# Kernel tuning notes

Measured on AMD Instinct MI355X. Metric: run time of the kernel, lower is better.

Reference implementation:

```python
import jax, jax.numpy as jnp
import numpy as np

BS, D = 8192, 128
SIGMA = 16.0

def setup_inputs() -> dict:
    key = jax.random.key(0)
    x = jax.random.normal(key, (BS, D), dtype=jnp.float32)
    return {"x": x}

def reference(x) -> jnp.ndarray:
    # kernel[j, i] = exp(-||x_i - x_j||^2 / (2 sigma^2))  (symmetric RBF Gram matrix)
    # Computed via the ||a-b||^2 = |a|^2 + |b|^2 - 2 a.b GEMM trick instead of the
    # original O(bs) loop of slice/sub/sum ops (same math, fused form).
    sq = jnp.sum(x * x, axis=1)                      # [bs]
    d2 = sq[:, None] + sq[None, :] - 2.0 * (x @ x.T)  # [bs, bs]
    d2 = jnp.maximum(d2, 0.0)                         # clamp tiny negative fp error
    kernel = jnp.exp(-d2 / (2.0 * SIGMA * SIGMA))
    # symmetric degree normalization: D^{-1/2} K D^{-1/2}
    ds = 1.0 / jnp.sqrt(jnp.sum(kernel, axis=0))      # [bs]
    return kernel * (ds[:, None] * ds[None, :])
```

## Files before the change

### kernel.cpp

```cpp
#include <hip/hip_runtime.h>
#include <hip/hip_bf16.h>

#define BSZ 8192
#define DIM 128

typedef __attribute__((ext_vector_type(8))) short bf16x8;
typedef __attribute__((ext_vector_type(4))) float f32x4;

__device__ __forceinline__ ushort f32_to_bf16(float f) {
    unsigned u = __float_as_uint(f);
    u += 0x7FFF + ((u >> 16) & 1);
    return (ushort)(u >> 16);
}

__global__ __launch_bounds__(256) void prep_kernel(const float* __restrict__ x,
                                                   ushort* __restrict__ xb,
                                                   float* __restrict__ sq) {
    const int wid  = threadIdx.x >> 6;
    const int lane = threadIdx.x & 63;
    const int g    = blockIdx.x * 4 + wid;
    const int fr   = lane & 15;
    const int kg   = lane >> 4;
    const int row  = g * 16 + fr;

    float s = 0.f;
    #pragma unroll
    for (int kk = 0; kk < 4; ++kk) {
        const float* p = x + (size_t)row * DIM + kk * 32 + kg * 8;
        const float4 v0 = *reinterpret_cast<const float4*>(p);
        const float4 v1 = *reinterpret_cast<const float4*>(p + 4);
        s += v0.x * v0.x + v0.y * v0.y + v0.z * v0.z + v0.w * v0.w;
        s += v1.x * v1.x + v1.y * v1.y + v1.z * v1.z + v1.w * v1.w;
        bf16x8 b;
        b[0] = (short)f32_to_bf16(v0.x); b[1] = (short)f32_to_bf16(v0.y);
        b[2] = (short)f32_to_bf16(v0.z); b[3] = (short)f32_to_bf16(v0.w);
        b[4] = (short)f32_to_bf16(v1.x); b[5] = (short)f32_to_bf16(v1.y);
        b[6] = (short)f32_to_bf16(v1.z); b[7] = (short)f32_to_bf16(v1.w);
        *reinterpret_cast<bf16x8*>(xb + ((size_t)(g * 4 + kk) * 64 + lane) * 8) = b;
    }
    s += __shfl_xor(s, 16);
    s += __shfl_xor(s, 32);
    if (lane < 16) sq[row] = s;
}

template <int PHASE>
__global__ __launch_bounds__(256) void rbf_kernel(const ushort* __restrict__ xb,
                                                  const float* __restrict__ sq,
                                                  float* __restrict__ colsum,
                                                  float* __restrict__ out) {
    const int lane = threadIdx.x & 63;
    const int wid  = threadIdx.x >> 6;
    const int fr   = lane & 15;
    const int kg   = lane >> 4;

    const int bx = blockIdx.x & 63;
    const int by = blockIdx.x >> 6;
    const int row0 = by * 128 + (wid >> 1) * 64;
    const int col0 = bx * 128 + (wid & 1) * 64;
    const int ga = row0 >> 4;
    const int gb = col0 >> 4;

    f32x4 acc[4][4];
    #pragma unroll
    for (int mi = 0; mi < 4; ++mi)
        #pragma unroll
        for (int ni = 0; ni < 4; ++ni)
            acc[mi][ni] = (f32x4){0.f, 0.f, 0.f, 0.f};

    #pragma unroll
    for (int kk = 0; kk < 4; ++kk) {
        bf16x8 a[4], b[4];
        #pragma unroll
        for (int mi = 0; mi < 4; ++mi)
            a[mi] = *reinterpret_cast<const bf16x8*>(
                xb + ((size_t)((ga + mi) * 4 + kk) * 64 + lane) * 8);
        #pragma unroll
        for (int ni = 0; ni < 4; ++ni)
            b[ni] = *reinterpret_cast<const bf16x8*>(
                xb + ((size_t)((gb + ni) * 4 + kk) * 64 + lane) * 8);
        #pragma unroll
        for (int mi = 0; mi < 4; ++mi)
            #pragma unroll
            for (int ni = 0; ni < 4; ++ni)
                acc[mi][ni] = __builtin_amdgcn_mfma_f32_16x16x32_bf16(a[mi], b[ni], acc[mi][ni], 0, 0, 0);
    }

    float sqr[4][4];
    #pragma unroll
    for (int mi = 0; mi < 4; ++mi) {
        const f32x4 t = *reinterpret_cast<const f32x4*>(sq + row0 + mi * 16 + kg * 4);
        #pragma unroll
        for (int r = 0; r < 4; ++r) sqr[mi][r] = t[r];
    }
    float sqc[4];
    #pragma unroll
    for (int ni = 0; ni < 4; ++ni) sqc[ni] = sq[col0 + ni * 16 + fr];

    const float inv = 1.0f / 512.0f;

    if (PHASE == 0) {
        float csum[4] = {0.f, 0.f, 0.f, 0.f};
        #pragma unroll
        for (int mi = 0; mi < 4; ++mi)
            #pragma unroll
            for (int ni = 0; ni < 4; ++ni)
                #pragma unroll
                for (int r = 0; r < 4; ++r) {
                    float t = fminf((2.f * acc[mi][ni][r] - sqr[mi][r] - sqc[ni]) * inv, 0.f);
                    csum[ni] += __expf(t);
                }
        #pragma unroll
        for (int ni = 0; ni < 4; ++ni) {
            csum[ni] += __shfl_xor(csum[ni], 16);
            csum[ni] += __shfl_xor(csum[ni], 32);
        }
        if (lane < 16) {
            #pragma unroll
            for (int ni = 0; ni < 4; ++ni)
                atomicAdd(&colsum[col0 + ni * 16 + fr], csum[ni]);
        }
    } else {
        float dsc[4];
        #pragma unroll
        for (int ni = 0; ni < 4; ++ni) dsc[ni] = rsqrtf(colsum[col0 + ni * 16 + fr]);
        float dsr[4][4];
        #pragma unroll
        for (int mi = 0; mi < 4; ++mi) {
            const f32x4 t = *reinterpret_cast<const f32x4*>(colsum + row0 + mi * 16 + kg * 4);
            #pragma unroll
            for (int r = 0; r < 4; ++r) dsr[mi][r] = rsqrtf(t[r]);
        }
        #pragma unroll
        for (int mi = 0; mi < 4; ++mi)
            #pragma unroll
            for (int ni = 0; ni < 4; ++ni)
                #pragma unroll
                for (int r = 0; r < 4; ++r) {
                    float t = fminf((2.f * acc[mi][ni][r] - sqr[mi][r] - sqc[ni]) * inv, 0.f);
                    float k = __expf(t);
                    const int row = row0 + mi * 16 + kg * 4 + r;
                    const int col = col0 + ni * 16 + fr;
                    __builtin_nontemporal_store(k * dsr[mi][r] * dsc[ni],
                                                &out[(size_t)row * BSZ + col]);
                }
    }
}

extern "C" void kernel_launch(void* const* d_in, const int* in_sizes, int n_in,
                              void* d_out, int out_size, void* d_ws, size_t ws_size,
                              hipStream_t stream) {
    const float* x = (const float*)d_in[0];
    float* out = (float*)d_out;

    ushort* xb    = (ushort*)d_ws;
    float* sq     = (float*)((char*)d_ws + (size_t)BSZ * DIM * 2);
    float* colsum = sq + BSZ;

    hipMemsetAsync(colsum, 0, BSZ * sizeof(float), stream);
    prep_kernel<<<512 / 4, 256, 0, stream>>>(x, xb, sq);
    rbf_kernel<0><<<64 * 64, 256, 0, stream>>>(xb, sq, colsum, out);
    rbf_kernel<1><<<64 * 64, 256, 0, stream>>>(xb, sq, colsum, out);
}
```

Measured before the change: 325.5 us.

## Exploit Gram symmetry for column sums and fold scale into exp2

The column-sum pass now covers only the upper-triangular 128x128 tiles (2080 blocks instead of 4096). Each block emits both column and row partial sums into a partial buffer, and a separate reduce kernel sums them, which replaces global atomics and the memset. The squared norms are prescaled by log2(e)/512 so the exponent becomes one fma plus exp2. This adds an extra kernel launch and a 64xBSZ partial buffer, and it relies on the bf16 GEMM giving row sums equal to column sums of the transposed tile.

```diff
diff --git a/kernel.cpp b/kernel.cpp
--- a/kernel.cpp
+++ b/kernel.cpp
@@ -3,6 +3,7 @@
 
 #define BSZ 8192
 #define DIM 128
+#define LOG2E 1.4426950408889634f
 
 typedef __attribute__((ext_vector_type(8))) short bf16x8;
 typedef __attribute__((ext_vector_type(4))) float f32x4;
@@ -15,7 +16,7 @@
 
 __global__ __launch_bounds__(256) void prep_kernel(const float* __restrict__ x,
                                                    ushort* __restrict__ xb,
-                                                   float* __restrict__ sq) {
+                                                   float* __restrict__ sq2) {
     const int wid  = threadIdx.x >> 6;
     const int lane = threadIdx.x & 63;
     const int g    = blockIdx.x * 4 + wid;
@@ -40,110 +41,182 @@
     }
     s += __shfl_xor(s, 16);
     s += __shfl_xor(s, 32);
-    if (lane < 16) sq[row] = s;
-}
-
-template <int PHASE>
-__global__ __launch_bounds__(256) void rbf_kernel(const ushort* __restrict__ xb,
-                                                  const float* __restrict__ sq,
-                                                  float* __restrict__ colsum,
-                                                  float* __restrict__ out) {
+    if (lane < 16) sq2[row] = s * (LOG2E / 512.f);
+}
+
+__device__ __forceinline__ void compute_tile(const ushort* __restrict__ xb,
+                                             int ga, int gb, int lane,
+                                             f32x4 (&acc)[4][4]) {
+    #pragma unroll
+    for (int mi = 0; mi < 4; ++mi)
+        #pragma unroll
+        for (int ni = 0; ni < 4; ++ni)
+            acc[mi][ni] = (f32x4){0.f, 0.f, 0.f, 0.f};
+    #pragma unroll
+    for (int kk = 0; kk < 4; ++kk) {
+        bf16x8 a[4], b[4];
+        #pragma unroll
+        for (int mi = 0; mi < 4; ++mi)
+            a[mi] = *reinterpret_cast<const bf16x8*>(
+                xb + ((size_t)((ga + mi) * 4 + kk) * 64 + lane) * 8);
+        #pragma unroll
+        for (int ni = 0; ni < 4; ++ni)
+            b[ni] = *reinterpret_cast<const bf16x8*>(
+                xb + ((size_t)((gb + ni) * 4 + kk) * 64 + lane) * 8);
+        #pragma unroll
+        for (int mi = 0; mi < 4; ++mi)
+            #pragma unroll
+            for (int ni = 0; ni < 4; ++ni)
+                acc[mi][ni] = __builtin_amdgcn_mfma_f32_16x16x32_bf16(a[mi], b[ni], acc[mi][ni], 0, 0, 0);
+    }
+}
+
+__global__ __launch_bounds__(256) void rbf_colsum(const ushort* __restrict__ xb,
+                                                  const float* __restrict__ sq2,
+                                                  float* __restrict__ part) {
+    const int t = blockIdx.x;
+    int bx = (int)((sqrtf(8.f * t + 1.f) - 1.f) * 0.5f);
+    while ((bx + 1) * (bx + 2) / 2 <= t) ++bx;
+    while (bx * (bx + 1) / 2 > t) --bx;
+    const int by = t - bx * (bx + 1) / 2;
+
     const int lane = threadIdx.x & 63;
     const int wid  = threadIdx.x >> 6;
     const int fr   = lane & 15;
     const int kg   = lane >> 4;
-
+    const int row0 = by * 128 + (wid >> 1) * 64;
+    const int col0 = bx * 128 + (wid & 1) * 64;
+
+    f32x4 acc[4][4];
+    compute_tile(xb, row0 >> 4, col0 >> 4, lane, acc);
+
+    float sq2r[4][4];
+    #pragma unroll
+    for (int mi = 0; mi < 4; ++mi) {
+        const f32x4 v = *reinterpret_cast<const f32x4*>(sq2 + row0 + mi * 16 + kg * 4);
+        #pragma unroll
+        for (int r = 0; r < 4; ++r) sq2r[mi][r] = v[r];
+    }
+    float sq2c[4];
+    #pragma unroll
+    for (int ni = 0; ni < 4; ++ni) sq2c[ni] = sq2[col0 + ni * 16 + fr];
+
+    const float C2 = LOG2E / 256.f;
+    float csum[4] = {0.f, 0.f, 0.f, 0.f};
+    float rsum[4][4];
+    #pragma unroll
+    for (int mi = 0; mi < 4; ++mi)
+        #pragma unroll
+        for (int r = 0; r < 4; ++r) rsum[mi][r] = 0.f;
+
+    #pragma unroll
+    for (int mi = 0; mi < 4; ++mi)
+        #pragma unroll
+        for (int ni = 0; ni < 4; ++ni)
+            #pragma unroll
+            for (int r = 0; r < 4; ++r) {
+                float tv = fminf(fmaf(acc[mi][ni][r], C2, -sq2r[mi][r]) - sq2c[ni], 0.f);
+                float e = __builtin_amdgcn_exp2f(tv);
+                csum[ni] += e;
+                rsum[mi][r] += e;
+            }
+
+    #pragma unroll
+    for (int ni = 0; ni < 4; ++ni) {
+        csum[ni] += __shfl_xor(csum[ni], 16);
+        csum[ni] += __shfl_xor(csum[ni], 32);
+    }
+    #pragma unroll
+    for (int mi = 0; mi < 4; ++mi)
+        #pragma unroll
+        for (int r = 0; r < 4; ++r) {
+            float v = rsum[mi][r];
+            v += __shfl_xor(v, 1);
+            v += __shfl_xor(v, 2);
+            v += __shfl_xor(v, 4);
+            v += __shfl_xor(v, 8);
+            rsum[mi][r] = v;
+        }
+
+    __shared__ float cs[128], rs[128];
+    if (threadIdx.x < 128) cs[threadIdx.x] = 0.f;
+    else rs[threadIdx.x - 128] = 0.f;
+    __syncthreads();
+    if (lane < 16) {
+        #pragma unroll
+        for (int ni = 0; ni < 4; ++ni)
+            atomicAdd(&cs[(wid & 1) * 64 + ni * 16 + fr], csum[ni]);
+    }
+    if (fr == 0) {
+        #pragma unroll
+        for (int mi = 0; mi < 4; ++mi)
+            #pragma unroll
+            for (int r = 0; r < 4; ++r)
+                atomicAdd(&rs[(wid >> 1) * 64 + mi * 16 + kg * 4 + r], rsum[mi][r]);
+    }
+    __syncthreads();
+    if (threadIdx.x < 128)
+        part[(size_t)by * BSZ + bx * 128 + threadIdx.x] = cs[threadIdx.x];
+    else if (by < bx)
+        part[(size_t)bx * BSZ + by * 128 + (threadIdx.x - 128)] = rs[threadIdx.x - 128];
+}
+
+__global__ __launch_bounds__(256) void reduce_colsum(const float* __restrict__ part,
+                                                     float* __restrict__ colsum) {
+    const int j = blockIdx.x * 256 + threadIdx.x;
+    float s = 0.f;
+    #pragma unroll
+    for (int a = 0; a < 64; ++a) s += part[(size_t)a * BSZ + j];
+    colsum[j] = s;
+}
+
+__global__ __launch_bounds__(256) void rbf_write(const ushort* __restrict__ xb,
+                                                 const float* __restrict__ sq2,
+                                                 const float* __restrict__ colsum,
+                                                 float* __restrict__ out) {
+    const int lane = threadIdx.x & 63;
+    const int wid  = threadIdx.x >> 6;
+    const int fr   = lane & 15;
+    const int kg   = lane >> 4;
     const int bx = blockIdx.x & 63;
     const int by = blockIdx.x >> 6;
     const int row0 = by * 128 + (wid >> 1) * 64;
     const int col0 = bx * 128 + (wid & 1) * 64;
-    const int ga = row0 >> 4;
-    const int gb = col0 >> 4;
 
     f32x4 acc[4][4];
-    #pragma unroll
-    for (int mi = 0; mi < 4; ++mi)
-        #pragma unroll
-        for (int ni = 0; ni < 4; ++ni)
-            acc[mi][ni] = (f32x4){0.f, 0.f, 0.f, 0.f};
-
-    #pragma unroll
-    for (int kk = 0; kk < 4; ++kk) {
-        bf16x8 a[4], b[4];
-        #pragma unroll
-        for (int mi = 0; mi < 4; ++mi)
-            a[mi] = *reinterpret_cast<const bf16x8*>(
-                xb + ((size_t)((ga + mi) * 4 + kk) * 64 + lane) * 8);
-        #pragma unroll
-        for (int ni = 0; ni < 4; ++ni)
-            b[ni] = *reinterpret_cast<const bf16x8*>(
-                xb + ((size_t)((gb + ni) * 4 + kk) * 64 + lane) * 8);
-        #pragma unroll
-        for (int mi = 0; mi < 4; ++mi)
-            #pragma unroll
-            for (int ni = 0; ni < 4; ++ni)
-                acc[mi][ni] = __builtin_amdgcn_mfma_f32_16x16x32_bf16(a[mi], b[ni], acc[mi][ni], 0, 0, 0);
-    }
-
-    float sqr[4][4];
+    compute_tile(xb, row0 >> 4, col0 >> 4, lane, acc);
+
+    float sq2r[4][4], dsr[4][4];
     #pragma unroll
     for (int mi = 0; mi < 4; ++mi) {
-        const f32x4 t = *reinterpret_cast<const f32x4*>(sq + row0 + mi * 16 + kg * 4);
-        #pragma unroll
-        for (int r = 0; r < 4; ++r) sqr[mi][r] = t[r];
-    }
-    float sqc[4];
-    #pragma unroll
-    for (int ni = 0; ni < 4; ++ni) sqc[ni] = sq[col0 + ni * 16 + fr];
-
-    const float inv = 1.0f / 512.0f;
-
-    if (PHASE == 0) {
-        float csum[4] = {0.f, 0.f, 0.f, 0.f};
-        #pragma unroll
-        for (int mi = 0; mi < 4; ++mi)
-            #pragma unroll
-            for (int ni = 0; ni < 4; ++ni)
-                #pragma unroll
-                for (int r = 0; r < 4; ++r) {
-                    float t = fminf((2.f * acc[mi][ni][r] - sqr[mi][r] - sqc[ni]) * inv, 0.f);
-                    csum[ni] += __expf(t);
-                }
+        const f32x4 v = *reinterpret_cast<const f32x4*>(sq2 + row0 + mi * 16 + kg * 4);
+        const f32x4 c = *reinterpret_cast<const f32x4*>(colsum + row0 + mi * 16 + kg * 4);
+        #pragma unroll
+        for (int r = 0; r < 4; ++r) { sq2r[mi][r] = v[r]; dsr[mi][r] = rsqrtf(c[r]); }
+    }
+    float sq2c[4], dsc[4];
+    #pragma unroll
+    for (int ni = 0; ni < 4; ++ni) {
+        sq2c[ni] = sq2[col0 + ni * 16 + fr];
+        dsc[ni]  = rsqrtf(colsum[col0 + ni * 16 + fr]);
+    }
+
+    const float C2 = LOG2E / 256.f;
+    #pragma unroll
+    for (int mi = 0; mi < 4; ++mi)
         #pragma unroll
         for (int ni = 0; ni < 4; ++ni) {
-            csum[ni] += __shfl_xor(csum[ni], 16);
-            csum[ni] += __shfl_xor(csum[ni], 32);
+            const float sc = dsc[ni];
+            #pragma unroll
+            for (int r = 0; r < 4; ++r) {
+                float tv = fminf(fmaf(acc[mi][ni][r], C2, -sq2r[mi][r]) - sq2c[ni], 0.f);
+                float e = __builtin_amdgcn_exp2f(tv);
+                const int row = row0 + mi * 16 + kg * 4 + r;
+                const int col = col0 + ni * 16 + fr;
+                __builtin_nontemporal_store(e * dsr[mi][r] * sc,
+                                            &out[(size_t)row * BSZ + col]);
+            }
         }
-        if (lane < 16) {
-            #pragma unroll
-            for (int ni = 0; ni < 4; ++ni)
-                atomicAdd(&colsum[col0 + ni * 16 + fr], csum[ni]);
-        }
-    } else {
-        float dsc[4];
-        #pragma unroll
-        for (int ni = 0; ni < 4; ++ni) dsc[ni] = rsqrtf(colsum[col0 + ni * 16 + fr]);
-        float dsr[4][4];
-        #pragma unroll
-        for (int mi = 0; mi < 4; ++mi) {
-            const f32x4 t = *reinterpret_cast<const f32x4*>(colsum + row0 + mi * 16 + kg * 4);
-            #pragma unroll
-            for (int r = 0; r < 4; ++r) dsr[mi][r] = rsqrtf(t[r]);
-        }
-        #pragma unroll
-        for (int mi = 0; mi < 4; ++mi)
-            #pragma unroll
-            for (int ni = 0; ni < 4; ++ni)
-                #pragma unroll
-                for (int r = 0; r < 4; ++r) {
-                    float t = fminf((2.f * acc[mi][ni][r] - sqr[mi][r] - sqc[ni]) * inv, 0.f);
-                    float k = __expf(t);
-                    const int row = row0 + mi * 16 + kg * 4 + r;
-                    const int col = col0 + ni * 16 + fr;
-                    __builtin_nontemporal_store(k * dsr[mi][r] * dsc[ni],
-                                                &out[(size_t)row * BSZ + col]);
-                }
-    }
 }
 
 extern "C" void kernel_launch(void* const* d_in, const int* in_sizes, int n_in,
@@ -153,11 +226,12 @@
     float* out = (float*)d_out;
 
     ushort* xb    = (ushort*)d_ws;
-    float* sq     = (float*)((char*)d_ws + (size_t)BSZ * DIM * 2);
-    float* colsum = sq + BSZ;
-
-    hipMemsetAsync(colsum, 0, BSZ * sizeof(float), stream);
-    prep_kernel<<<512 / 4, 256, 0, stream>>>(x, xb, sq);
-    rbf_kernel<0><<<64 * 64, 256, 0, stream>>>(xb, sq, colsum, out);
-    rbf_kernel<1><<<64 * 64, 256, 0, stream>>>(xb, sq, colsum, out);
-}
+    float* sq2    = (float*)((char*)d_ws + (size_t)BSZ * DIM * 2);
+    float* colsum = sq2 + BSZ;
+    float* part   = colsum + BSZ;
+
+    prep_kernel<<<512 / 4, 256, 0, stream>>>(x, xb, sq2);
+    rbf_colsum<<<2080, 256, 0, stream>>>(xb, sq2, part);
+    reduce_colsum<<<BSZ / 256, 256, 0, stream>>>(part, colsum);
+    rbf_write<<<64 * 64, 256, 0, stream>>>(xb, sq2, colsum, out);
+}
```

New measurement: 336.6 us. 1.03x slower.
